# Performance work log

Hardware: AMD Instinct MI355X
Metric: run time of the kernel (lower is better)

Reference implementation:

```python
import jax, jax.numpy as jnp
import numpy as np

D, H, K, L, F, G, M, OUT = 1280, 16, 80, 4, 5120, 48, 2, 2048
HALF = K // 2  # rotary half dim = 40


def _token_coords(grid_thw, merge_size, N):
    tpi = grid_thw[:, 0] * grid_thw[:, 1] * grid_thw[:, 2]
    cu = jnp.concatenate([jnp.zeros(1, jnp.int32), jnp.cumsum(tpi).astype(jnp.int32)])
    tok = jnp.arange(N, dtype=jnp.int32)
    img_id = jnp.searchsorted(cu[1:], tok, side='right')
    local = tok - cu[img_id]
    h = grid_thw[img_id, 1]
    w = grid_thw[img_id, 2]
    spatial = local % (h * w)
    msq = merge_size * merge_size
    mw = w // merge_size
    group, intra = spatial // msq, spatial % msq
    row = (group // mw) * merge_size + intra // merge_size
    col = (group % mw) * merge_size + intra % merge_size
    return row, col, h, w, cu


def _layernorm(x, s, b, eps=1e-6):
    mu = jnp.mean(x, -1, keepdims=True)
    var = jnp.mean(jnp.square(x - mu), -1, keepdims=True)
    return (x - mu) * jax.lax.rsqrt(var + eps) * s + b


def _rotate_half(x):
    x1, x2 = x[..., :HALF], x[..., HALF:]
    return jnp.concatenate([-x2, x1], axis=-1)


def setup_inputs() -> dict:
    key = jax.random.key(0)
    ks = jax.random.split(key, 16)
    s = 0.02
    inp = {
        'pixels': jax.random.normal(ks[0], (2048, 1536), jnp.float32),
        'grid_thw': jnp.array([[1, 16, 32]] * 4, jnp.int32),
        'pos_embed': jax.random.normal(ks[1], (G * G, D), jnp.float32) * s,
        'patch_w': jax.random.normal(ks[2], (1536, D), jnp.float32) * s,
        'patch_b': jnp.zeros((D,), jnp.float32),
        'ln1_s': jnp.ones((L, D), jnp.float32), 'ln1_b': jnp.zeros((L, D), jnp.float32),
        'qkv_w': jax.random.normal(ks[3], (L, D, 3 * D), jnp.float32) * s,
        'qkv_b': jnp.zeros((L, 3 * D), jnp.float32),
        'proj_w': jax.random.normal(ks[4], (L, D, D), jnp.float32) * s,
        'proj_b': jnp.zeros((L, D), jnp.float32),
        'ln2_s': jnp.ones((L, D), jnp.float32), 'ln2_b': jnp.zeros((L, D), jnp.float32),
        'fc1_w': jax.random.normal(ks[5], (L, D, F), jnp.float32) * s,
        'fc1_b': jnp.zeros((L, F), jnp.float32),
        'fc2_w': jax.random.normal(ks[6], (L, F, D), jnp.float32) * s,
        'fc2_b': jnp.zeros((L, D), jnp.float32),
        'm_norm_s': jnp.ones((D,), jnp.float32), 'm_norm_b': jnp.zeros((D,), jnp.float32),
        'm_fc1_w': jax.random.normal(ks[7], (D * M * M, D * M * M), jnp.float32) * s,
        'm_fc1_b': jnp.zeros((D * M * M,), jnp.float32),
        'm_fc2_w': jax.random.normal(ks[8], (D * M * M, OUT), jnp.float32) * s,
        'm_fc2_b': jnp.zeros((OUT,), jnp.float32),
    }
    return inp


def _forward(pixels, grid_thw, pos_embed, patch_w, patch_b, ln1_s, ln1_b, qkv_w, qkv_b,
             proj_w, proj_b, ln2_s, ln2_b, fc1_w, fc1_b, fc2_w, fc2_b,
             m_norm_s, m_norm_b, m_fc1_w, m_fc1_b, m_fc2_w, m_fc2_b):
    N = pixels.shape[0]
    row, col, h, w, cu = _token_coords(grid_thw, M, N)

    # patch embed: conv with stride==kernel over flattened patches == linear
    x = pixels @ patch_w + patch_b  # [N, D]

    # bilinear position-embedding interpolation onto each image's (h, w) grid
    rf = jnp.where(h > 1, row.astype(jnp.float32) * (G - 1) / jnp.maximum(h - 1, 1), 0.0)
    cf = jnp.where(w > 1, col.astype(jnp.float32) * (G - 1) / jnp.maximum(w - 1, 1), 0.0)
    r0 = jnp.floor(rf).astype(jnp.int32); r1 = jnp.minimum(r0 + 1, G - 1)
    c0 = jnp.floor(cf).astype(jnp.int32); c1 = jnp.minimum(c0 + 1, G - 1)
    wr = (rf - r0)[:, None]; wc = (cf - c0)[:, None]
    pe = (pos_embed[r0 * G + c0] * (1 - wr) * (1 - wc)
          + pos_embed[r0 * G + c1] * (1 - wr) * wc
          + pos_embed[r1 * G + c0] * wr * (1 - wc)
          + pos_embed[r1 * G + c1] * wr * wc)
    x = x + pe

    # 2-D rotary embeddings
    inv_freq = 1.0 / (10000.0 ** (jnp.arange(0, HALF, 2, dtype=jnp.float32) / HALF))
    freqs = jnp.concatenate([row[:, None].astype(jnp.float32) * inv_freq,
                             col[:, None].astype(jnp.float32) * inv_freq], axis=-1)  # [N, HALF]
    emb = jnp.concatenate([freqs, freqs], axis=-1)  # [N, K]
    cos, sin = jnp.cos(emb)[:, None, :], jnp.sin(emb)[:, None, :]  # [N,1,K]

    # block-diagonal segment mask via cu_seqlens (N is a multiple of 128; no pad)
    tok = jnp.arange(N)
    seg = jnp.searchsorted(cu[1:], tok, side='right')
    k_start = cu[jnp.minimum(seg, cu.shape[0] - 2)]
    k_end = cu[jnp.minimum(seg + 1, cu.shape[0] - 1)]
    mask = (tok[None, :] >= k_start[:, None]) & (tok[None, :] < k_end[:, None])  # [N,N]
    scale = K ** -0.5

    for l in range(L):
        hdn = _layernorm(x, ln1_s[l], ln1_b[l])
        qkv = (hdn @ qkv_w[l] + qkv_b[l]).reshape(N, 3, H, K)
        q, k, v = qkv[:, 0], qkv[:, 1], qkv[:, 2]
        q = q * cos + _rotate_half(q) * sin
        k = k * cos + _rotate_half(k) * sin
        scores = jnp.einsum('nhk,mhk->hnm', q, k) * scale
        scores = jnp.where(mask[None], scores, jnp.finfo(scores.dtype).min)
        attn = jax.nn.softmax(scores, axis=-1)
        o = jnp.einsum('hnm,mhk->nhk', attn, v).reshape(N, D)
        x = x + o @ proj_w[l] + proj_b[l]

        hdn = _layernorm(x, ln2_s[l], ln2_b[l])
        ff = jax.nn.gelu(hdn @ fc1_w[l] + fc1_b[l], approximate=True)
        x = x + ff @ fc2_w[l] + fc2_b[l]

    # patch merger
    normed = _layernorm(x, m_norm_s, m_norm_b).reshape(N // (M * M), D * M * M)
    ff = jax.nn.gelu(normed @ m_fc1_w + m_fc1_b, approximate=True)
    return ff @ m_fc2_w + m_fc2_b  # [N/4, OUT]


def reference(pixels, grid_thw, pos_embed, patch_w, patch_b, ln1_s, ln1_b, qkv_w, qkv_b,
              proj_w, proj_b, ln2_s, ln2_b, fc1_w, fc1_b, fc2_w, fc2_b,
              m_norm_s, m_norm_b, m_fc1_w, m_fc1_b, m_fc2_w, m_fc2_b):
    return _forward(pixels, grid_thw, pos_embed, patch_w, patch_b, ln1_s, ln1_b, qkv_w, qkv_b,
                    proj_w, proj_b, ln2_s, ln2_b, fc1_w, fc1_b, fc2_w, fc2_b,
                    m_norm_s, m_norm_b, m_fc1_w, m_fc1_b, m_fc2_w, m_fc2_b)
```

## Files before the change

### kernel.cpp

```cpp
#include <hip/hip_runtime.h>
#include <math.h>

#define DMODEL 1280
#define NHEADS 16
#define FDIM   5120
#define GPOS   48
#define SEG    512

typedef __attribute__((ext_vector_type(8))) short bf16x8;
typedef __attribute__((ext_vector_type(4))) float f32x4;
typedef unsigned short u16;

__device__ __forceinline__ u16 f2bf(float f) {
  unsigned int u = __float_as_uint(f);
  u = (u + 0x7FFFu + ((u >> 16) & 1u)) >> 16;
  return (u16)u;
}
__device__ __forceinline__ float bf2f(u16 u) {
  return __uint_as_float((unsigned int)u << 16);
}
__device__ __forceinline__ float gelu_tanh(float x) {
  float u = 0.7978845608028654f * (x + 0.044715f * x * x * x);
  float t = __expf(2.f * u);
  float th = 1.f - 2.f / (t + 1.f);
  return 0.5f * x * (1.f + th);
}

typedef const __attribute__((address_space(1))) unsigned int* gas_t;
typedef __attribute__((address_space(3))) unsigned int* las_t;
__device__ __forceinline__ void async16(const void* g, void* l) {
  __builtin_amdgcn_global_load_lds((gas_t)g, (las_t)l, 16, 0, 0);
}

__device__ __forceinline__ int xcd_remap(int b, int nwg) {
  int q = nwg >> 3, r = nwg & 7, x = b & 7, d = b >> 3;
  return (x < r ? x * (q + 1) : r * (q + 1) + (x - r) * q) + d;
}

#define STG1(mat, PW, ldx, rb, kk, pp)                                      \
  async16((PW) + (long long)(rb) * 16 * (ldx) + (kk),                       \
          &L[pp][mat][(rb) * 512])

#define BARX() asm volatile("s_barrier" ::: "memory")
#define LGKM0() asm volatile("s_waitcnt lgkmcnt(0)" ::: "memory")

template <int EPI>
__global__ __launch_bounds__(256, 3) void gemm128(
    const u16* __restrict__ A, const u16* __restrict__ B,
    const float* __restrict__ bias, void* __restrict__ Cv,
    int Kd, int lda, int ldb, int ldc, int nsplit, long long pstride) {
  __shared__ __align__(16) u16 L[2][2][4096];
  const int sp = blockIdx.z;
  const int Ks = Kd / nsplit;
  const int NT = Ks >> 5;
  const u16* Ab = A + (long long)sp * Ks;
  const u16* Bb = B + (long long)sp * Ks;
  const int gx = gridDim.x;
  const int lg = xcd_remap(blockIdx.x + gx * blockIdx.y, gx * gridDim.y);
  const int m0 = (lg % gx) * 128, n0 = (lg / gx) * 128;
  const int t = threadIdx.x, ln = t & 63, w = t >> 6;
  const int wr = w >> 1, wc = w & 1;
  const int m16 = ln & 15, q = ln >> 4;
  const int r16 = ln >> 2;
  const int csw = (ln & 3) ^ ((ln >> 5) << 1);
  const int rbase = m16 * 32 + (q ^ ((m16 >> 3) << 1)) * 8;

  const u16* Aw = Ab + (long long)(m0 + r16) * lda + csw * 8;
  const u16* Bw = Bb + (long long)(n0 + r16) * ldb + csw * 8;
  const int w4 = w + 4;

  f32x4 acc[4][4];
#pragma unroll
  for (int i = 0; i < 4; i++)
#pragma unroll
    for (int j = 0; j < 4; j++)
#pragma unroll
      for (int r = 0; r < 4; r++) acc[i][j][r] = 0.f;

  STG1(0, Aw, lda, w, 0, 0);  STG1(0, Aw, lda, w4, 0, 0);
  STG1(1, Bw, ldb, w, 0, 0);  STG1(1, Bw, ldb, w4, 0, 0);
  if (NT > 1) {
    STG1(0, Aw, lda, w, 32, 1);  STG1(0, Aw, lda, w4, 32, 1);
    STG1(1, Bw, ldb, w, 32, 1);  STG1(1, Bw, ldb, w4, 32, 1);
    asm volatile("s_waitcnt vmcnt(4)" ::: "memory");
  } else {
    asm volatile("s_waitcnt vmcnt(0)" ::: "memory");
  }
  BARX();

  for (int tt = 0; tt < NT; ++tt) {
    const int p = tt & 1;
    const u16* Abuf = &L[p][0][0];
    const u16* Bbuf = &L[p][1][0];
    bf16x8 aR[4], bR[4];

#pragma unroll
    for (int i = 0; i < 4; ++i)
      aR[i] = *(const bf16x8*)(Abuf + (wr * 4 + i) * 512 + rbase);
    bR[0] = *(const bf16x8*)(Bbuf + (wc * 4 + 0) * 512 + rbase);
    bR[1] = *(const bf16x8*)(Bbuf + (wc * 4 + 1) * 512 + rbase);
    if (tt + 1 < NT) {
      STG1(0, Aw, lda, w, (tt + 1) * 32, p ^ 1);
      STG1(0, Aw, lda, w4, (tt + 1) * 32, p ^ 1);
    }
    BARX();
    LGKM0();
    __builtin_amdgcn_s_setprio(1);
#pragma unroll
    for (int i = 0; i < 4; ++i) {
      acc[i][0] = __builtin_amdgcn_mfma_f32_16x16x32_bf16(aR[i], bR[0], acc[i][0], 0, 0, 0);
      acc[i][1] = __builtin_amdgcn_mfma_f32_16x16x32_bf16(aR[i], bR[1], acc[i][1], 0, 0, 0);
    }
    __builtin_amdgcn_s_setprio(0);
    BARX();

    bR[2] = *(const bf16x8*)(Bbuf + (wc * 4 + 2) * 512 + rbase);
    bR[3] = *(const bf16x8*)(Bbuf + (wc * 4 + 3) * 512 + rbase);
    if (tt + 1 < NT) {
      STG1(1, Bw, ldb, w, (tt + 1) * 32, p ^ 1);
      STG1(1, Bw, ldb, w4, (tt + 1) * 32, p ^ 1);
    }
    BARX();
    LGKM0();
    __builtin_amdgcn_s_setprio(1);
#pragma unroll
    for (int i = 0; i < 4; ++i) {
      acc[i][2] = __builtin_amdgcn_mfma_f32_16x16x32_bf16(aR[i], bR[2], acc[i][2], 0, 0, 0);
      acc[i][3] = __builtin_amdgcn_mfma_f32_16x16x32_bf16(aR[i], bR[3], acc[i][3], 0, 0, 0);
    }
    __builtin_amdgcn_s_setprio(0);
    if (tt + 1 < NT) asm volatile("s_waitcnt vmcnt(0)" ::: "memory");
    BARX();
  }

#pragma unroll
  for (int fr = 0; fr < 4; fr++) {
#pragma unroll
    for (int r = 0; r < 4; r++) {
      int row = m0 + wr * 64 + fr * 16 + q * 4 + r;
      if (EPI == 0) {
        u16* Cp = (u16*)Cv + (long long)sp * pstride + (long long)row * ldc;
#pragma unroll
        for (int fc = 0; fc < 4; fc++)
          Cp[n0 + wc * 64 + fc * 16 + m16] = f2bf(acc[fr][fc][r]);
      } else if (EPI == 1) {
        u16* Cb = (u16*)Cv + (long long)row * ldc;
#pragma unroll
        for (int fc = 0; fc < 4; fc++) {
          int col = n0 + wc * 64 + fc * 16 + m16;
          Cb[col] = f2bf(acc[fr][fc][r] + bias[col]);
        }
      } else {
        u16* Cb = (u16*)Cv + (long long)row * ldc;
#pragma unroll
        for (int fc = 0; fc < 4; fc++) {
          int col = n0 + wc * 64 + fc * 16 + m16;
          Cb[col] = f2bf(gelu_tanh(acc[fr][fc][r] + bias[col]));
        }
      }
    }
  }
}

__global__ __launch_bounds__(512) void fattn_k(
    const u16* __restrict__ qr, const u16* __restrict__ kr,
    const u16* __restrict__ vpT, u16* __restrict__ o, int N, float iscale) {
  __shared__ __align__(16) u16 Ks[2][24][512];
  __shared__ __align__(16) u16 Vs[2][20][512];
  __shared__ __align__(16) u16 Ps[8][16 * 128];
  const int nseg = N >> 9;
  const int gx = gridDim.x;
  const int lg = xcd_remap(blockIdx.x + gx * blockIdx.y, gx * gridDim.y);
  const int strip = lg % gx, hb = lg / gx;
  const int h = hb / nseg, seg = hb - h * nseg;
  const int t = threadIdx.x, ln = t & 63, w = t >> 6;
  const int m16 = ln & 15, qh = ln >> 4;
  const int r4 = ln >> 2, gsw = (ln & 3) ^ ((ln >> 5) << 1);
  const int rbase = m16 * 32 + ((qh ^ ((m16 >> 3) << 1)) << 3);
  const long long hN = (long long)h * N;
  const int segbase = seg * SEG;
  const int q0 = segbase + strip * 128 + w * 16;

  bf16x8 qf[3];
#pragma unroll
  for (int ks = 0; ks < 3; ks++)
    qf[ks] = *(const bf16x8*)&qr[(hN + q0 + m16) * 96 + ks * 32 + qh * 8];

  f32x4 ao[5];
#pragma unroll
  for (int df = 0; df < 5; df++)
#pragma unroll
    for (int r = 0; r < 4; r++) ao[df][r] = 0.f;
  float m_[4], l_[4];
#pragma unroll
  for (int r = 0; r < 4; r++) { m_[r] = -1e30f; l_[r] = 0.f; }

  auto stage = [&](int c, int pb) {
#pragma unroll
    for (int i = 0; i < 3; i++) {
      int sK = w * 3 + i, f = sK / 3, kg = sK - f * 3;
      async16(&kr[(hN + segbase + c * 128 + f * 16 + r4) * 96 + kg * 32 + gsw * 8],
              &Ks[pb][sK][0]);
    }
#pragma unroll
    for (int i = 0; i < 2; i++) {
      int sV = w * 2 + i, df = sV >> 2, kvg = sV & 3;
      async16(&vpT[((long long)hb * 128 + df * 16 + r4) * SEG + c * 128 + kvg * 32 + gsw * 8],
              &Vs[pb][sV][0]);
    }
    if (w < 4) {
      int sV = 16 + w, df = sV >> 2, kvg = sV & 3;
      async16(&vpT[((long long)hb * 128 + df * 16 + r4) * SEG + c * 128 + kvg * 32 + gsw * 8],
              &Vs[pb][sV][0]);
    }
  };

  stage(0, 0);
  u16* Pmy = &Ps[w][0];
  for (int c = 0; c < 4; c++) {
    const int pb = c & 1;
    __syncthreads();
    if (c < 3) stage(c + 1, pb ^ 1);

    f32x4 s[8];
#pragma unroll
    for (int f = 0; f < 8; f++)
#pragma unroll
      for (int r = 0; r < 4; r++) s[f][r] = 0.f;
#pragma unroll
    for (int ks = 0; ks < 3; ks++) {
#pragma unroll
      for (int f = 0; f < 8; f++) {
        bf16x8 kf = *(const bf16x8*)&Ks[pb][f * 3 + ks][rbase];
        s[f] = __builtin_amdgcn_mfma_f32_16x16x32_bf16(qf[ks], kf, s[f], 0, 0, 0);
      }
    }

#pragma unroll
    for (int r = 0; r < 4; r++) {
      float mx = s[0][r];
#pragma unroll
      for (int f = 1; f < 8; f++) mx = fmaxf(mx, s[f][r]);
      mx *= iscale;
#pragma unroll
      for (int o2 = 1; o2 <= 8; o2 <<= 1) mx = fmaxf(mx, __shfl_xor(mx, o2));
      float mn = fmaxf(m_[r], mx);
      float corr = __expf(m_[r] - mn);
      m_[r] = mn;
      float rs = 0.f;
#pragma unroll
      for (int f = 0; f < 8; f++) {
        float p = __expf(s[f][r] * iscale - mn);
        s[f][r] = p;
        rs += p;
      }
#pragma unroll
      for (int o2 = 1; o2 <= 8; o2 <<= 1) rs += __shfl_xor(rs, o2);
      l_[r] = l_[r] * corr + rs;
#pragma unroll
      for (int df = 0; df < 5; df++) ao[df][r] *= corr;
    }

#pragma unroll
    for (int r = 0; r < 4; r++) {
      int qq = qh * 4 + r;
      int base = qq * 128 + (m16 & 7);
      int ql = qq & 7;
#pragma unroll
      for (int f = 0; f < 8; f++) {
        int gr = (f * 2 + (m16 >> 3)) ^ ql;
        Pmy[base + gr * 8] = f2bf(s[f][r]);
      }
    }

#pragma unroll
    for (int ks = 0; ks < 4; ks++) {
      bf16x8 pf = *(const bf16x8*)&Pmy[m16 * 128 +
                                       (((ks * 4 + qh) ^ (m16 & 7)) << 3)];
#pragma unroll
      for (int df = 0; df < 5; df++) {
        bf16x8 vf = *(const bf16x8*)&Vs[pb][df * 4 + ks][rbase];
        ao[df] = __builtin_amdgcn_mfma_f32_16x16x32_bf16(pf, vf, ao[df], 0, 0, 0);
      }
    }
  }

#pragma unroll
  for (int r = 0; r < 4; r++) {
    float rl = 1.f / l_[r];
    long long rowb = (long long)(q0 + qh * 4 + r) * DMODEL + h * 80;
#pragma unroll
    for (int df = 0; df < 5; df++)
      o[rowb + df * 16 + m16] = f2bf(ao[df][r] * rl);
  }
}

template <int S, int RES, int GELU, int OUTBF>
__global__ void reduce_k(const u16* __restrict__ Pp, long long mn, int Nn,
                         const float* __restrict__ bias,
                         const float* __restrict__ res, void* __restrict__ out) {
  long long i = ((long long)blockIdx.x * 256 + threadIdx.x) * 4;
  if (i >= mn) return;
  float vx = 0.f, vy = 0.f, vz = 0.f, vw = 0.f;
#pragma unroll
  for (int s = 0; s < S; s++) {
    ushort4 u4 = *(const ushort4*)(Pp + (long long)s * mn + i);
    vx += bf2f(u4.x); vy += bf2f(u4.y); vz += bf2f(u4.z); vw += bf2f(u4.w);
  }
  int col = (int)(i % Nn);
  vx += bias[col]; vy += bias[col + 1]; vz += bias[col + 2]; vw += bias[col + 3];
  if (GELU) {
    vx = gelu_tanh(vx); vy = gelu_tanh(vy);
    vz = gelu_tanh(vz); vw = gelu_tanh(vw);
  }
  if (RES) {
    float4 r4 = *(const float4*)(res + i);
    vx += r4.x; vy += r4.y; vz += r4.z; vw += r4.w;
  }
  if (OUTBF) {
    ushort4 o; o.x = f2bf(vx); o.y = f2bf(vy); o.z = f2bf(vz); o.w = f2bf(vw);
    *(ushort4*)((u16*)out + i) = o;
  } else {
    float4 o; o.x = vx; o.y = vy; o.z = vz; o.w = vw;
    *(float4*)((float*)out + i) = o;
  }
}

template <int S>
__global__ void redln_k(const u16* __restrict__ Pp, long long mn,
                        const float* __restrict__ bias,
                        float* __restrict__ x,
                        const float* __restrict__ s, const float* __restrict__ b,
                        u16* __restrict__ h) {
  int row = blockIdx.x;
  int d = threadIdx.x * 4;
  long long base = (long long)row * DMODEL + d;
  float vx = 0.f, vy = 0.f, vz = 0.f, vw = 0.f;
#pragma unroll
  for (int si = 0; si < S; si++) {
    ushort4 u4 = *(const ushort4*)(Pp + (long long)si * mn + base);
    vx += bf2f(u4.x); vy += bf2f(u4.y); vz += bf2f(u4.z); vw += bf2f(u4.w);
  }
  vx += bias[d]; vy += bias[d + 1]; vz += bias[d + 2]; vw += bias[d + 3];
  float4 r4 = *(const float4*)(x + base);
  vx += r4.x; vy += r4.y; vz += r4.z; vw += r4.w;
  float4 xv; xv.x = vx; xv.y = vy; xv.z = vz; xv.w = vw;
  *(float4*)(x + base) = xv;
  float sum = vx + vy + vz + vw;
#pragma unroll
  for (int o = 32; o; o >>= 1) sum += __shfl_xor(sum, o);
  __shared__ float red[8];
  int wv = threadIdx.x >> 6, lnn = threadIdx.x & 63;
  if (lnn == 0) red[wv] = sum;
  __syncthreads();
  float mu = 0.f;
  for (int i = 0; i < 5; i++) mu += red[i];
  mu *= (1.f / DMODEL);
  float dx = vx - mu, dy = vy - mu, dz = vz - mu, dw = vw - mu;
  float s2 = dx * dx + dy * dy + dz * dz + dw * dw;
#pragma unroll
  for (int o = 32; o; o >>= 1) s2 += __shfl_xor(s2, o);
  __syncthreads();
  if (lnn == 0) red[wv] = s2;
  __syncthreads();
  float var = 0.f;
  for (int i = 0; i < 5; i++) var += red[i];
  var *= (1.f / DMODEL);
  float rs = rsqrtf(var + 1e-6f);
  ushort4 o4;
  o4.x = f2bf(dx * rs * s[d] + b[d]);
  o4.y = f2bf(dy * rs * s[d + 1] + b[d + 1]);
  o4.z = f2bf(dz * rs * s[d + 2] + b[d + 2]);
  o4.w = f2bf(dw * rs * s[d + 3] + b[d + 3]);
  *(ushort4*)(h + base) = o4;
}

union U16x8 { uint4 v; u16 s[8]; };
__global__ void wconv_k(const float* __restrict__ in, u16* __restrict__ out,
                        int K, int N) {
  __shared__ float tl[64][33];
  int n0 = blockIdx.x * 32, k0 = blockIdx.y * 64;
  int t = threadIdx.x;
  int rr = t >> 5, c = t & 31;
#pragma unroll
  for (int i = 0; i < 8; i++)
    tl[rr + 8 * i][c] = in[(long long)(k0 + rr + 8 * i) * N + n0 + c];
  __syncthreads();
  int n = t >> 3, kq = (t & 7) * 8;
  U16x8 o;
#pragma unroll
  for (int j = 0; j < 8; j++) o.s[j] = f2bf(tl[kq + j][n]);
  *(uint4*)&out[(long long)(n0 + n) * K + k0 + kq] = o.v;
}

__global__ void conv_k(const float* __restrict__ in, u16* __restrict__ out,
                       long long n) {
  long long i = ((long long)blockIdx.x * 256 + threadIdx.x) * 4;
  if (i >= n) return;
  float4 v = *(const float4*)(in + i);
  ushort4 o; o.x = f2bf(v.x); o.y = f2bf(v.y); o.z = f2bf(v.z); o.w = f2bf(v.w);
  *(ushort4*)&out[i] = o;
}

__global__ void vtr_k(const u16* __restrict__ in, u16* __restrict__ out) {
  __shared__ u16 tl[64][65];
  int b = blockIdx.z;
  int m0 = blockIdx.x * 64;
  int d0 = blockIdx.y * 64;
  const u16* ib = in + (long long)b * SEG * 128;
  u16* ob = out + (long long)b * 128 * SEG;
  int t = threadIdx.x;
  int r = t >> 3, c8 = (t & 7) * 8;
#pragma unroll
  for (int i = 0; i < 2; i++) {
    U16x8 ld;
    ld.v = *(const uint4*)&ib[(long long)(m0 + r + 32 * i) * 128 + d0 + c8];
#pragma unroll
    for (int j = 0; j < 8; j++) tl[r + 32 * i][c8 + j] = ld.s[j];
  }
  __syncthreads();
  int d = t >> 3, m8 = (t & 7) * 8;
#pragma unroll
  for (int i = 0; i < 2; i++) {
    int dd = d + 32 * i;
    U16x8 st;
#pragma unroll
    for (int j = 0; j < 8; j++) st.s[j] = tl[m8 + j][dd];
    *(uint4*)&ob[(long long)(d0 + dd) * SEG + m0 + m8] = st.v;
  }
}

__global__ void coords_k(const int* __restrict__ g, int nimg,
                         int* __restrict__ rw, int* __restrict__ cl,
                         int* __restrict__ hh, int* __restrict__ ww, int N) {
  int t = blockIdx.x * 256 + threadIdx.x;
  if (t >= N) return;
  int c = 0, local = 0, H = 1, W = 1;
  for (int i = 0; i < nimg; i++) {
    int tpi = g[i * 3] * g[i * 3 + 1] * g[i * 3 + 2];
    if (t >= c && t < c + tpi) { local = t - c; H = g[i * 3 + 1]; W = g[i * 3 + 2]; }
    c += tpi;
  }
  int hw = H * W;
  int sp = local % hw;
  int mw = W >> 1;
  int gr = sp >> 2, intra = sp & 3;
  rw[t] = (gr / mw) * 2 + (intra >> 1);
  cl[t] = (gr % mw) * 2 + (intra & 1);
  hh[t] = H; ww[t] = W;
}

__global__ void peadd_k(float* __restrict__ x, const float* __restrict__ pe,
                        const int* __restrict__ rw, const int* __restrict__ cl,
                        const int* __restrict__ hh, const int* __restrict__ ww) {
  int n = blockIdx.x;
  int d = threadIdx.x * 4;
  int H = hh[n], W = ww[n];
  float rf = (H > 1) ? (float)rw[n] * (float)(GPOS - 1) / (float)(H - 1) : 0.f;
  float cf = (W > 1) ? (float)cl[n] * (float)(GPOS - 1) / (float)(W - 1) : 0.f;
  int r0 = (int)floorf(rf), c0 = (int)floorf(cf);
  int r1 = min(r0 + 1, GPOS - 1), c1 = min(c0 + 1, GPOS - 1);
  float wr = rf - (float)r0, wc = cf - (float)c0;
  float w00 = (1.f - wr) * (1.f - wc), w01 = (1.f - wr) * wc;
  float w10 = wr * (1.f - wc), w11 = wr * wc;
  float4 v00 = *(const float4*)(pe + (long long)(r0 * GPOS + c0) * DMODEL + d);
  float4 v01 = *(const float4*)(pe + (long long)(r0 * GPOS + c1) * DMODEL + d);
  float4 v10 = *(const float4*)(pe + (long long)(r1 * GPOS + c0) * DMODEL + d);
  float4 v11 = *(const float4*)(pe + (long long)(r1 * GPOS + c1) * DMODEL + d);
  float4 xv = *(float4*)(x + (long long)n * DMODEL + d);
  xv.x += w00 * v00.x + w01 * v01.x + w10 * v10.x + w11 * v11.x;
  xv.y += w00 * v00.y + w01 * v01.y + w10 * v10.y + w11 * v11.y;
  xv.z += w00 * v00.z + w01 * v01.z + w10 * v10.z + w11 * v11.z;
  xv.w += w00 * v00.w + w01 * v01.w + w10 * v10.w + w11 * v11.w;
  *(float4*)(x + (long long)n * DMODEL + d) = xv;
}

__global__ void ln_k(const float* __restrict__ X, u16* __restrict__ Y,
                     const float* __restrict__ s, const float* __restrict__ b) {
  int row = blockIdx.x;
  int d = threadIdx.x * 4;
  const float* x = X + (long long)row * DMODEL;
  float4 v = *(const float4*)(x + d);
  float sum = v.x + v.y + v.z + v.w;
#pragma unroll
  for (int o = 32; o; o >>= 1) sum += __shfl_xor(sum, o);
  __shared__ float red[8];
  int wv = threadIdx.x >> 6, lnn = threadIdx.x & 63;
  if (lnn == 0) red[wv] = sum;
  __syncthreads();
  float mu = 0.f;
  for (int i = 0; i < 5; i++) mu += red[i];
  mu *= (1.f / DMODEL);
  float dx = v.x - mu, dy = v.y - mu, dz = v.z - mu, dw = v.w - mu;
  float s2 = dx * dx + dy * dy + dz * dz + dw * dw;
#pragma unroll
  for (int o = 32; o; o >>= 1) s2 += __shfl_xor(s2, o);
  __syncthreads();
  if (lnn == 0) red[wv] = s2;
  __syncthreads();
  float var = 0.f;
  for (int i = 0; i < 5; i++) var += red[i];
  var *= (1.f / DMODEL);
  float rs = rsqrtf(var + 1e-6f);
  ushort4 o4;
  o4.x = f2bf(dx * rs * s[d] + b[d]);
  o4.y = f2bf(dy * rs * s[d + 1] + b[d + 1]);
  o4.z = f2bf(dz * rs * s[d + 2] + b[d + 2]);
  o4.w = f2bf(dw * rs * s[d + 3] + b[d + 3]);
  *(ushort4*)(Y + (long long)row * DMODEL + d) = o4;
}

__global__ void rope_k(const u16* __restrict__ qkv, const int* __restrict__ rw,
                       const int* __restrict__ cl, u16* __restrict__ qr,
                       u16* __restrict__ kr, u16* __restrict__ vp, int N) {
  int n = blockIdx.x * 4 + (threadIdx.x >> 6), h = blockIdx.y;
  int t = threadIdx.x & 63;
  const u16* src = qkv + (long long)n * (3 * DMODEL) + h * 80;
  long long ob96 = ((long long)h * N + n) * 96;
  long long ob128 = ((long long)h * N + n) * 128;
  if (t < 40) {
    float pos = (t < 20) ? (float)rw[n] : (float)cl[n];
    float infr = exp2f(-13.287712379549449f * (float)(t % 20) * 0.05f);
    float f = pos * infr;
    float cs = cosf(f), sn = sinf(f);
    float q0 = bf2f(src[t]), q1 = bf2f(src[t + 40]);
    qr[ob96 + t] = f2bf(q0 * cs - q1 * sn);
    qr[ob96 + t + 40] = f2bf(q1 * cs + q0 * sn);
    float k0 = bf2f(src[DMODEL + t]), k1 = bf2f(src[DMODEL + t + 40]);
    kr[ob96 + t] = f2bf(k0 * cs - k1 * sn);
    kr[ob96 + t + 40] = f2bf(k1 * cs + k0 * sn);
    vp[ob128 + t] = src[2 * DMODEL + t];
    vp[ob128 + t + 40] = src[2 * DMODEL + t + 40];
  } else {
    int u = t - 40;
    if (u < 16) { qr[ob96 + 80 + u] = 0; kr[ob96 + 80 + u] = 0; }
    vp[ob128 + 80 + u] = 0;
    vp[ob128 + 104 + u] = 0;
  }
}

static void gemm_big(hipStream_t st, int epi, const u16* A, const u16* B,
                     const float* bias, void* C, int M, int Nn, int Kd,
                     int lda, int ldb, int ldc, int nsplit) {
  dim3 g(M / 128, Nn / 128, nsplit), blk(256);
  long long ps = (long long)M * Nn;
  switch (epi) {
    case 0: gemm128<0><<<g, blk, 0, st>>>(A, B, bias, C, Kd, lda, ldb, ldc, nsplit, ps); break;
    case 1: gemm128<1><<<g, blk, 0, st>>>(A, B, bias, C, Kd, lda, ldb, ldc, nsplit, ps); break;
    default: gemm128<3><<<g, blk, 0, st>>>(A, B, bias, C, Kd, lda, ldb, ldc, nsplit, ps); break;
  }
}

extern "C" void kernel_launch(void* const* d_in, const int* in_sizes, int n_in,
                              void* d_out, int out_size, void* d_ws, size_t ws_size,
                              hipStream_t stream) {
  const float* pixels = (const float*)d_in[0];
  const int* grid_thw = (const int*)d_in[1];
  const float* pos_embed = (const float*)d_in[2];
  const float* patch_w = (const float*)d_in[3];
  const float* patch_b = (const float*)d_in[4];
  const float* ln1_s = (const float*)d_in[5];
  const float* ln1_b = (const float*)d_in[6];
  const float* qkv_w = (const float*)d_in[7];
  const float* qkv_b = (const float*)d_in[8];
  const float* proj_w = (const float*)d_in[9];
  const float* proj_b = (const float*)d_in[10];
  const float* ln2_s = (const float*)d_in[11];
  const float* ln2_b = (const float*)d_in[12];
  const float* fc1_w = (const float*)d_in[13];
  const float* fc1_b = (const float*)d_in[14];
  const float* fc2_w = (const float*)d_in[15];
  const float* fc2_b = (const float*)d_in[16];
  const float* mns = (const float*)d_in[17];
  const float* mnb = (const float*)d_in[18];
  const float* mf1w = (const float*)d_in[19];
  const float* mf1b = (const float*)d_in[20];
  const float* mf2w = (const float*)d_in[21];
  const float* mf2b = (const float*)d_in[22];
  float* out = (float*)d_out;

  const int N = in_sizes[0] / 1536;
  const int nimg = in_sizes[1] / 3;
  const int nseg = N / SEG;
  const int nb = NHEADS * nseg;

  char* w = (char*)d_ws;
  size_t off = 0;
  auto alloc = [&](size_t bytes) -> void* {
    void* p = w + off;
    off += (bytes + 255) & ~(size_t)255;
    return p;
  };
  int* rw = (int*)alloc((size_t)N * 4);
  int* cl = (int*)alloc((size_t)N * 4);
  int* hh = (int*)alloc((size_t)N * 4);
  int* ww = (int*)alloc((size_t)N * 4);
  float* x = (float*)alloc((size_t)N * DMODEL * 4);
  u16* h = (u16*)alloc((size_t)N * DMODEL * 2);
  u16* pixbf = (u16*)alloc((size_t)N * 1536 * 2);
  u16* patchT = (u16*)alloc((size_t)DMODEL * 1536 * 2);
  u16* qkvT = (u16*)alloc((size_t)3 * DMODEL * DMODEL * 2);
  u16* projT = (u16*)alloc((size_t)DMODEL * DMODEL * 2);
  u16* fc1T = (u16*)alloc((size_t)FDIM * DMODEL * 2);
  u16* fc2T = (u16*)alloc((size_t)DMODEL * FDIM * 2);
  u16* qkvb = (u16*)alloc((size_t)N * 3 * DMODEL * 2);
  u16* qr = (u16*)alloc((size_t)NHEADS * N * 96 * 2);
  u16* kr = (u16*)alloc((size_t)NHEADS * N * 96 * 2);
  u16* vp = (u16*)alloc((size_t)NHEADS * N * 128 * 2);
  u16* vpT = (u16*)alloc((size_t)NHEADS * N * 128 * 2);
  u16* pad0 = (u16*)alloc((size_t)nb * 2 * SEG * 128 * 2);
  u16* o = (u16*)alloc((size_t)N * DMODEL * 2);
  float* bigA = (float*)alloc((size_t)nb * SEG * SEG * 4);
  float* bigB = (float*)alloc((size_t)nb * SEG * SEG * 2);
  (void)ws_size; (void)pad0;
  u16* mfc1T = qkvb;
  u16* mfc2T = pixbf;
  u16* ffb = (u16*)bigA;
  u16* mf = (u16*)bigA;
  u16* part = (u16*)bigB;

  const float iscale = 0.11180339887498949f;
  const long long mnD = (long long)N * DMODEL;

  coords_k<<<dim3((N + 255) / 256), 256, 0, stream>>>(grid_thw, nimg, rw, cl, hh, ww, N);
  conv_k<<<dim3((int)(((long long)N * 1536 / 4 + 255) / 256)), 256, 0, stream>>>(
      pixels, pixbf, (long long)N * 1536);
  wconv_k<<<dim3(DMODEL / 32, 1536 / 64), 256, 0, stream>>>(patch_w, patchT, 1536, DMODEL);
  gemm_big(stream, 0, pixbf, patchT, nullptr, part, N, DMODEL, 1536, 1536, 1536,
           DMODEL, 4);
  reduce_k<4, 0, 0, 0><<<dim3((int)((mnD / 4 + 255) / 256)), 256, 0, stream>>>(
      part, mnD, DMODEL, patch_b, nullptr, x);
  peadd_k<<<dim3(N), 320, 0, stream>>>(x, pos_embed, rw, cl, hh, ww);
  ln_k<<<dim3(N), 320, 0, stream>>>(x, h, ln1_s, ln1_b);

  for (int l = 0; l < 4; l++) {
    wconv_k<<<dim3(3 * DMODEL / 32, DMODEL / 64), 256, 0, stream>>>(
        qkv_w + (size_t)l * DMODEL * 3 * DMODEL, qkvT, DMODEL, 3 * DMODEL);
    wconv_k<<<dim3(DMODEL / 32, DMODEL / 64), 256, 0, stream>>>(
        proj_w + (size_t)l * DMODEL * DMODEL, projT, DMODEL, DMODEL);
    wconv_k<<<dim3(FDIM / 32, DMODEL / 64), 256, 0, stream>>>(
        fc1_w + (size_t)l * DMODEL * FDIM, fc1T, DMODEL, FDIM);
    wconv_k<<<dim3(DMODEL / 32, FDIM / 64), 256, 0, stream>>>(
        fc2_w + (size_t)l * FDIM * DMODEL, fc2T, FDIM, DMODEL);

    gemm_big(stream, 1, h, qkvT, qkv_b + (size_t)l * 3 * DMODEL, qkvb, N,
             3 * DMODEL, DMODEL, DMODEL, DMODEL, 3 * DMODEL, 1);
    rope_k<<<dim3(N / 4, NHEADS), 256, 0, stream>>>(qkvb, rw, cl, qr, kr, vp, N);
    vtr_k<<<dim3(8, 2, nb), 256, 0, stream>>>(vp, vpT);
    fattn_k<<<dim3(SEG / 128, nb), 512, 0, stream>>>(qr, kr, vpT, o, N, iscale);
    gemm_big(stream, 0, o, projT, nullptr, part, N, DMODEL, DMODEL, DMODEL,
             DMODEL, DMODEL, 4);
    redln_k<4><<<dim3(N), 320, 0, stream>>>(part, mnD, proj_b + (size_t)l * DMODEL,
                                            x, ln2_s + (size_t)l * DMODEL,
                                            ln2_b + (size_t)l * DMODEL, h);
    gemm_big(stream, 3, h, fc1T, fc1_b + (size_t)l * FDIM, ffb, N, FDIM, DMODEL,
             DMODEL, DMODEL, FDIM, 1);
    gemm_big(stream, 0, ffb, fc2T, nullptr, part, N, DMODEL, FDIM, FDIM, FDIM,
             DMODEL, 4);
    const float* nsl = (l < 3) ? ln1_s + (size_t)(l + 1) * DMODEL : mns;
    const float* nbl = (l < 3) ? ln1_b + (size_t)(l + 1) * DMODEL : mnb;
    redln_k<4><<<dim3(N), 320, 0, stream>>>(part, mnD, fc2_b + (size_t)l * DMODEL,
                                            x, nsl, nbl, h);
  }

  const int Mm = N / 4;
  wconv_k<<<dim3(FDIM / 32, FDIM / 64), 256, 0, stream>>>(mf1w, mfc1T, FDIM, FDIM);
  gemm_big(stream, 0, h, mfc1T, nullptr, part, Mm, FDIM, FDIM, FDIM, FDIM, FDIM, 4);
  reduce_k<4, 0, 1, 1><<<dim3((int)(((long long)Mm * FDIM / 4 + 255) / 256)), 256, 0, stream>>>(
      part, (long long)Mm * FDIM, FDIM, mf1b, nullptr, mf);
  wconv_k<<<dim3(2048 / 32, FDIM / 64), 256, 0, stream>>>(mf2w, mfc2T, FDIM, 2048);
  gemm_big(stream, 0, mf, mfc2T, nullptr, part, Mm, 2048, FDIM, FDIM, FDIM, 2048, 16);
  reduce_k<16, 0, 0, 0><<<dim3((int)(((long long)Mm * 2048 / 4 + 255) / 256)), 256, 0, stream>>>(
      part, (long long)Mm * 2048, 2048, mf2b, nullptr, out);
}
```

Before: 1.311 ms.

## Shrink attention blocks to 256 threads and fuse patch reduce, pos-embed and layernorm

The attention kernel now uses 4 warps per block covering 64 queries. It drops the double-buffered K/V shared-memory staging in favour of a single buffer loaded synchronously per chunk, and launches twice as many blocks. This lowers shared memory per block and may raise occupancy, at the cost of losing overlap between loads and MFMA work. Separately, the patch-embedding split-K reduction, positional-embedding interpolation and first layernorm are merged into one kernel, removing two launches and a round trip of x through memory.

```diff
diff --git a/kernel.cpp b/kernel.cpp
--- a/kernel.cpp
+++ b/kernel.cpp
@@ -162,12 +162,12 @@
   }
 }
 
-__global__ __launch_bounds__(512) void fattn_k(
+__global__ __launch_bounds__(256) void fattn_k(
     const u16* __restrict__ qr, const u16* __restrict__ kr,
     const u16* __restrict__ vpT, u16* __restrict__ o, int N, float iscale) {
-  __shared__ __align__(16) u16 Ks[2][24][512];
-  __shared__ __align__(16) u16 Vs[2][20][512];
-  __shared__ __align__(16) u16 Ps[8][16 * 128];
+  __shared__ __align__(16) u16 Ks[24][512];
+  __shared__ __align__(16) u16 Vs[20][512];
+  __shared__ __align__(16) u16 Ps[4][16 * 128];
   const int nseg = N >> 9;
   const int gx = gridDim.x;
   const int lg = xcd_remap(blockIdx.x + gx * blockIdx.y, gx * gridDim.y);
@@ -179,7 +179,7 @@
   const int rbase = m16 * 32 + ((qh ^ ((m16 >> 3) << 1)) << 3);
   const long long hN = (long long)h * N;
   const int segbase = seg * SEG;
-  const int q0 = segbase + strip * 128 + w * 16;
+  const int q0 = segbase + strip * 64 + w * 16;
 
   bf16x8 qf[3];
 #pragma unroll
@@ -195,32 +195,26 @@
 #pragma unroll
   for (int r = 0; r < 4; r++) { m_[r] = -1e30f; l_[r] = 0.f; }
 
-  auto stage = [&](int c, int pb) {
-#pragma unroll
-    for (int i = 0; i < 3; i++) {
-      int sK = w * 3 + i, f = sK / 3, kg = sK - f * 3;
+  auto stage = [&](int c) {
+#pragma unroll
+    for (int i = 0; i < 6; i++) {
+      int sK = w * 6 + i, f = sK / 3, kg = sK - f * 3;
       async16(&kr[(hN + segbase + c * 128 + f * 16 + r4) * 96 + kg * 32 + gsw * 8],
-              &Ks[pb][sK][0]);
-    }
-#pragma unroll
-    for (int i = 0; i < 2; i++) {
-      int sV = w * 2 + i, df = sV >> 2, kvg = sV & 3;
+              &Ks[sK][0]);
+    }
+#pragma unroll
+    for (int i = 0; i < 5; i++) {
+      int sV = w * 5 + i, df = sV >> 2, kvg = sV & 3;
       async16(&vpT[((long long)hb * 128 + df * 16 + r4) * SEG + c * 128 + kvg * 32 + gsw * 8],
-              &Vs[pb][sV][0]);
-    }
-    if (w < 4) {
-      int sV = 16 + w, df = sV >> 2, kvg = sV & 3;
-      async16(&vpT[((long long)hb * 128 + df * 16 + r4) * SEG + c * 128 + kvg * 32 + gsw * 8],
-              &Vs[pb][sV][0]);
+              &Vs[sV][0]);
     }
   };
 
-  stage(0, 0);
   u16* Pmy = &Ps[w][0];
   for (int c = 0; c < 4; c++) {
-    const int pb = c & 1;
+    if (c) __syncthreads();
+    stage(c);
     __syncthreads();
-    if (c < 3) stage(c + 1, pb ^ 1);
 
     f32x4 s[8];
 #pragma unroll
@@ -231,7 +225,7 @@
     for (int ks = 0; ks < 3; ks++) {
 #pragma unroll
       for (int f = 0; f < 8; f++) {
-        bf16x8 kf = *(const bf16x8*)&Ks[pb][f * 3 + ks][rbase];
+        bf16x8 kf = *(const bf16x8*)&Ks[f * 3 + ks][rbase];
         s[f] = __builtin_amdgcn_mfma_f32_16x16x32_bf16(qf[ks], kf, s[f], 0, 0, 0);
       }
     }
@@ -279,7 +273,7 @@
                                        (((ks * 4 + qh) ^ (m16 & 7)) << 3)];
 #pragma unroll
       for (int df = 0; df < 5; df++) {
-        bf16x8 vf = *(const bf16x8*)&Vs[pb][df * 4 + ks][rbase];
+        bf16x8 vf = *(const bf16x8*)&Vs[df * 4 + ks][rbase];
         ao[df] = __builtin_amdgcn_mfma_f32_16x16x32_bf16(pf, vf, ao[df], 0, 0, 0);
       }
     }
@@ -375,86 +369,24 @@
   *(ushort4*)(h + base) = o4;
 }
 
-union U16x8 { uint4 v; u16 s[8]; };
-__global__ void wconv_k(const float* __restrict__ in, u16* __restrict__ out,
-                        int K, int N) {
-  __shared__ float tl[64][33];
-  int n0 = blockIdx.x * 32, k0 = blockIdx.y * 64;
-  int t = threadIdx.x;
-  int rr = t >> 5, c = t & 31;
-#pragma unroll
-  for (int i = 0; i < 8; i++)
-    tl[rr + 8 * i][c] = in[(long long)(k0 + rr + 8 * i) * N + n0 + c];
-  __syncthreads();
-  int n = t >> 3, kq = (t & 7) * 8;
-  U16x8 o;
-#pragma unroll
-  for (int j = 0; j < 8; j++) o.s[j] = f2bf(tl[kq + j][n]);
-  *(uint4*)&out[(long long)(n0 + n) * K + k0 + kq] = o.v;
-}
-
-__global__ void conv_k(const float* __restrict__ in, u16* __restrict__ out,
-                       long long n) {
-  long long i = ((long long)blockIdx.x * 256 + threadIdx.x) * 4;
-  if (i >= n) return;
-  float4 v = *(const float4*)(in + i);
-  ushort4 o; o.x = f2bf(v.x); o.y = f2bf(v.y); o.z = f2bf(v.z); o.w = f2bf(v.w);
-  *(ushort4*)&out[i] = o;
-}
-
-__global__ void vtr_k(const u16* __restrict__ in, u16* __restrict__ out) {
-  __shared__ u16 tl[64][65];
-  int b = blockIdx.z;
-  int m0 = blockIdx.x * 64;
-  int d0 = blockIdx.y * 64;
-  const u16* ib = in + (long long)b * SEG * 128;
-  u16* ob = out + (long long)b * 128 * SEG;
-  int t = threadIdx.x;
-  int r = t >> 3, c8 = (t & 7) * 8;
-#pragma unroll
-  for (int i = 0; i < 2; i++) {
-    U16x8 ld;
-    ld.v = *(const uint4*)&ib[(long long)(m0 + r + 32 * i) * 128 + d0 + c8];
-#pragma unroll
-    for (int j = 0; j < 8; j++) tl[r + 32 * i][c8 + j] = ld.s[j];
-  }
-  __syncthreads();
-  int d = t >> 3, m8 = (t & 7) * 8;
-#pragma unroll
-  for (int i = 0; i < 2; i++) {
-    int dd = d + 32 * i;
-    U16x8 st;
-#pragma unroll
-    for (int j = 0; j < 8; j++) st.s[j] = tl[m8 + j][dd];
-    *(uint4*)&ob[(long long)(d0 + dd) * SEG + m0 + m8] = st.v;
-  }
-}
-
-__global__ void coords_k(const int* __restrict__ g, int nimg,
-                         int* __restrict__ rw, int* __restrict__ cl,
-                         int* __restrict__ hh, int* __restrict__ ww, int N) {
-  int t = blockIdx.x * 256 + threadIdx.x;
-  if (t >= N) return;
-  int c = 0, local = 0, H = 1, W = 1;
-  for (int i = 0; i < nimg; i++) {
-    int tpi = g[i * 3] * g[i * 3 + 1] * g[i * 3 + 2];
-    if (t >= c && t < c + tpi) { local = t - c; H = g[i * 3 + 1]; W = g[i * 3 + 2]; }
-    c += tpi;
-  }
-  int hw = H * W;
-  int sp = local % hw;
-  int mw = W >> 1;
-  int gr = sp >> 2, intra = sp & 3;
-  rw[t] = (gr / mw) * 2 + (intra >> 1);
-  cl[t] = (gr % mw) * 2 + (intra & 1);
-  hh[t] = H; ww[t] = W;
-}
-
-__global__ void peadd_k(float* __restrict__ x, const float* __restrict__ pe,
-                        const int* __restrict__ rw, const int* __restrict__ cl,
-                        const int* __restrict__ hh, const int* __restrict__ ww) {
+__global__ void redpeln_k(const u16* __restrict__ Pp, long long mn,
+                          const float* __restrict__ bias,
+                          const float* __restrict__ pe,
+                          const int* __restrict__ rw, const int* __restrict__ cl,
+                          const int* __restrict__ hh, const int* __restrict__ ww,
+                          float* __restrict__ x,
+                          const float* __restrict__ s, const float* __restrict__ b,
+                          u16* __restrict__ h) {
   int n = blockIdx.x;
   int d = threadIdx.x * 4;
+  long long base = (long long)n * DMODEL + d;
+  float vx = 0.f, vy = 0.f, vz = 0.f, vw = 0.f;
+#pragma unroll
+  for (int si = 0; si < 4; si++) {
+    ushort4 u4 = *(const ushort4*)(Pp + (long long)si * mn + base);
+    vx += bf2f(u4.x); vy += bf2f(u4.y); vz += bf2f(u4.z); vw += bf2f(u4.w);
+  }
+  vx += bias[d]; vy += bias[d + 1]; vz += bias[d + 2]; vw += bias[d + 3];
   int H = hh[n], W = ww[n];
   float rf = (H > 1) ? (float)rw[n] * (float)(GPOS - 1) / (float)(H - 1) : 0.f;
   float cf = (W > 1) ? (float)cl[n] * (float)(GPOS - 1) / (float)(W - 1) : 0.f;
@@ -467,21 +399,13 @@
   float4 v01 = *(const float4*)(pe + (long long)(r0 * GPOS + c1) * DMODEL + d);
   float4 v10 = *(const float4*)(pe + (long long)(r1 * GPOS + c0) * DMODEL + d);
   float4 v11 = *(const float4*)(pe + (long long)(r1 * GPOS + c1) * DMODEL + d);
-  float4 xv = *(float4*)(x + (long long)n * DMODEL + d);
-  xv.x += w00 * v00.x + w01 * v01.x + w10 * v10.x + w11 * v11.x;
-  xv.y += w00 * v00.y + w01 * v01.y + w10 * v10.y + w11 * v11.y;
-  xv.z += w00 * v00.z + w01 * v01.z + w10 * v10.z + w11 * v11.z;
-  xv.w += w00 * v00.w + w01 * v01.w + w10 * v10.w + w11 * v11.w;
-  *(float4*)(x + (long long)n * DMODEL + d) = xv;
-}
-
-__global__ void ln_k(const float* __restrict__ X, u16* __restrict__ Y,
-                     const float* __restrict__ s, const float* __restrict__ b) {
-  int row = blockIdx.x;
-  int d = threadIdx.x * 4;
-  const float* x = X + (long long)row * DMODEL;
-  float4 v = *(const float4*)(x + d);
-  float sum = v.x + v.y + v.z + v.w;
+  vx += w00 * v00.x + w01 * v01.x + w10 * v10.x + w11 * v11.x;
+  vy += w00 * v00.y + w01 * v01.y + w10 * v10.y + w11 * v11.y;
+  vz += w00 * v00.z + w01 * v01.z + w10 * v10.z + w11 * v11.z;
+  vw += w00 * v00.w + w01 * v01.w + w10 * v10.w + w11 * v11.w;
+  float4 xv; xv.x = vx; xv.y = vy; xv.z = vz; xv.w = vw;
+  *(float4*)(x + base) = xv;
+  float sum = vx + vy + vz + vw;
 #pragma unroll
   for (int o = 32; o; o >>= 1) sum += __shfl_xor(sum, o);
   __shared__ float red[8];
@@ -491,7 +415,7 @@
   float mu = 0.f;
   for (int i = 0; i < 5; i++) mu += red[i];
   mu *= (1.f / DMODEL);
-  float dx = v.x - mu, dy = v.y - mu, dz = v.z - mu, dw = v.w - mu;
+  float dx = vx - mu, dy = vy - mu, dz = vz - mu, dw = vw - mu;
   float s2 = dx * dx + dy * dy + dz * dz + dw * dw;
 #pragma unroll
   for (int o = 32; o; o >>= 1) s2 += __shfl_xor(s2, o);
@@ -507,7 +431,82 @@
   o4.y = f2bf(dy * rs * s[d + 1] + b[d + 1]);
   o4.z = f2bf(dz * rs * s[d + 2] + b[d + 2]);
   o4.w = f2bf(dw * rs * s[d + 3] + b[d + 3]);
-  *(ushort4*)(Y + (long long)row * DMODEL + d) = o4;
+  *(ushort4*)(h + base) = o4;
+}
+
+union U16x8 { uint4 v; u16 s[8]; };
+__global__ void wconv_k(const float* __restrict__ in, u16* __restrict__ out,
+                        int K, int N) {
+  __shared__ float tl[64][33];
+  int n0 = blockIdx.x * 32, k0 = blockIdx.y * 64;
+  int t = threadIdx.x;
+  int rr = t >> 5, c = t & 31;
+#pragma unroll
+  for (int i = 0; i < 8; i++)
+    tl[rr + 8 * i][c] = in[(long long)(k0 + rr + 8 * i) * N + n0 + c];
+  __syncthreads();
+  int n = t >> 3, kq = (t & 7) * 8;
+  U16x8 o;
+#pragma unroll
+  for (int j = 0; j < 8; j++) o.s[j] = f2bf(tl[kq + j][n]);
+  *(uint4*)&out[(long long)(n0 + n) * K + k0 + kq] = o.v;
+}
+
+__global__ void conv_k(const float* __restrict__ in, u16* __restrict__ out,
+                       long long n) {
+  long long i = ((long long)blockIdx.x * 256 + threadIdx.x) * 4;
+  if (i >= n) return;
+  float4 v = *(const float4*)(in + i);
+  ushort4 o; o.x = f2bf(v.x); o.y = f2bf(v.y); o.z = f2bf(v.z); o.w = f2bf(v.w);
+  *(ushort4*)&out[i] = o;
+}
+
+__global__ void vtr_k(const u16* __restrict__ in, u16* __restrict__ out) {
+  __shared__ u16 tl[64][65];
+  int b = blockIdx.z;
+  int m0 = blockIdx.x * 64;
+  int d0 = blockIdx.y * 64;
+  const u16* ib = in + (long long)b * SEG * 128;
+  u16* ob = out + (long long)b * 128 * SEG;
+  int t = threadIdx.x;
+  int r = t >> 3, c8 = (t & 7) * 8;
+#pragma unroll
+  for (int i = 0; i < 2; i++) {
+    U16x8 ld;
+    ld.v = *(const uint4*)&ib[(long long)(m0 + r + 32 * i) * 128 + d0 + c8];
+#pragma unroll
+    for (int j = 0; j < 8; j++) tl[r + 32 * i][c8 + j] = ld.s[j];
+  }
+  __syncthreads();
+  int d = t >> 3, m8 = (t & 7) * 8;
+#pragma unroll
+  for (int i = 0; i < 2; i++) {
+    int dd = d + 32 * i;
+    U16x8 st;
+#pragma unroll
+    for (int j = 0; j < 8; j++) st.s[j] = tl[m8 + j][dd];
+    *(uint4*)&ob[(long long)(d0 + dd) * SEG + m0 + m8] = st.v;
+  }
+}
+
+__global__ void coords_k(const int* __restrict__ g, int nimg,
+                         int* __restrict__ rw, int* __restrict__ cl,
+                         int* __restrict__ hh, int* __restrict__ ww, int N) {
+  int t = blockIdx.x * 256 + threadIdx.x;
+  if (t >= N) return;
+  int c = 0, local = 0, H = 1, W = 1;
+  for (int i = 0; i < nimg; i++) {
+    int tpi = g[i * 3] * g[i * 3 + 1] * g[i * 3 + 2];
+    if (t >= c && t < c + tpi) { local = t - c; H = g[i * 3 + 1]; W = g[i * 3 + 2]; }
+    c += tpi;
+  }
+  int hw = H * W;
+  int sp = local % hw;
+  int mw = W >> 1;
+  int gr = sp >> 2, intra = sp & 3;
+  rw[t] = (gr / mw) * 2 + (intra >> 1);
+  cl[t] = (gr % mw) * 2 + (intra & 1);
+  hh[t] = H; ww[t] = W;
 }
 
 __global__ void rope_k(const u16* __restrict__ qkv, const int* __restrict__ rw,
@@ -628,10 +627,8 @@
   wconv_k<<<dim3(DMODEL / 32, 1536 / 64), 256, 0, stream>>>(patch_w, patchT, 1536, DMODEL);
   gemm_big(stream, 0, pixbf, patchT, nullptr, part, N, DMODEL, 1536, 1536, 1536,
            DMODEL, 4);
-  reduce_k<4, 0, 0, 0><<<dim3((int)((mnD / 4 + 255) / 256)), 256, 0, stream>>>(
-      part, mnD, DMODEL, patch_b, nullptr, x);
-  peadd_k<<<dim3(N), 320, 0, stream>>>(x, pos_embed, rw, cl, hh, ww);
-  ln_k<<<dim3(N), 320, 0, stream>>>(x, h, ln1_s, ln1_b);
+  redpeln_k<<<dim3(N), 320, 0, stream>>>(part, mnD, patch_b, pos_embed,
+                                         rw, cl, hh, ww, x, ln1_s, ln1_b, h);
 
   for (int l = 0; l < 4; l++) {
     wconv_k<<<dim3(3 * DMODEL / 32, DMODEL / 64), 256, 0, stream>>>(
@@ -647,7 +644,7 @@
              3 * DMODEL, DMODEL, DMODEL, DMODEL, 3 * DMODEL, 1);
     rope_k<<<dim3(N / 4, NHEADS), 256, 0, stream>>>(qkvb, rw, cl, qr, kr, vp, N);
     vtr_k<<<dim3(8, 2, nb), 256, 0, stream>>>(vp, vpT);
-    fattn_k<<<dim3(SEG / 128, nb), 512, 0, stream>>>(qr, kr, vpT, o, N, iscale);
+    fattn_k<<<dim3(8, nb), 256, 0, stream>>>(qr, kr, vpT, o, N, iscale);
     gemm_big(stream, 0, o, projT, nullptr, part, N, DMODEL, DMODEL, DMODEL,
              DMODEL, DMODEL, 4);
     redln_k<4><<<dim3(N), 320, 0, stream>>>(part, mnD, proj_b + (size_t)l * DMODEL,
```

Result: no change. 1.307 ms (-0.3%).
